# Optimization experiments

Measured on AMD Instinct MI355X. Metric: run time of the kernel, lower is better.

## Reference

```python
import jax, jax.numpy as jnp
import numpy as np
import math

D_K = 64

def setup_inputs() -> dict:
    key = jax.random.key(0)
    k1, k2, k3, k4 = jax.random.split(key, 4)
    B, H, S, D = 2, 16, 2048, D_K
    query = jax.random.normal(k1, (B, H, S, D), dtype=jnp.float32)
    kk = jax.random.normal(k2, (B, H, S, D), dtype=jnp.float32)
    value = jax.random.normal(k3, (B, H, S, D), dtype=jnp.float32)
    mask = jax.random.randint(k4, (B, 1, S, S), 0, 2).astype(bool)
    return {"query": query, "key": kk, "value": value, "mask": mask}

def reference(query, key, value, mask):
    # score = Q K^T / sqrt(d_k)  -> [B,H,S,S]
    score = jnp.einsum('bhqd,bhkd->bhqk', query, key) * (1.0 / math.sqrt(D_K))
    # masked_fill(mask, -inf)
    score = jnp.where(mask, -jnp.inf, score)
    attn = jax.nn.softmax(score, axis=-1)
    # rows that are fully masked produce NaN -> 0 (torch.nan_to_num)
    attn = jnp.nan_to_num(attn, nan=0.0)
    # dropout with drop_rate=0 is identity
    return jnp.einsum('bhqk,bhkd->bhqd', attn, value)
```

## Files before the change

### kernel.cpp

```cpp
#include <hip/hip_runtime.h>
#include <hip/hip_bf16.h>


#define S_LEN 2048
#define D_DIM 64
#define BH    32
#define BM    64
#define BN    64
#define PST   72
#define QSCALE 0.1803368801f

typedef __bf16    bf16_t;
typedef _Float16  f16_t;
typedef bf16_t bf16x8 __attribute__((ext_vector_type(8)));
typedef f16_t  f16x4  __attribute__((ext_vector_type(4)));
typedef float  f32x4  __attribute__((ext_vector_type(4)));
typedef unsigned char  u8;
typedef unsigned long long u64b;

__device__ __forceinline__ void load_lds16(const void* g, void* l) {
    __builtin_amdgcn_global_load_lds(
        (const __attribute__((address_space(1))) void*)g,
        (__attribute__((address_space(3))) void*)l, 16, 0, 0);
}

__global__ __launch_bounds__(256)
void mask_to_bits(const unsigned* __restrict__ M, u64b* __restrict__ bm)
{
    const int t = threadIdx.x;
    unsigned p = M[(t * 8179) & ((1 << 21) - 1)];
    const int is_u8 = __syncthreads_or(p > 1u);
    const int id = blockIdx.x * 256 + t;
    u64b w = 0;
    if (is_u8) {
        const uint4* src = (const uint4*)((const u8*)M + (size_t)id * 64);
        #pragma unroll
        for (int g = 0; g < 4; ++g) {
            uint4 x = src[g];
            const unsigned dw[4] = {x.x, x.y, x.z, x.w};
            #pragma unroll
            for (int q = 0; q < 4; ++q) {
                const unsigned v = dw[q];
                const int base = g * 16 + q * 4;
                if (v & 0x000000FFu) w |= 1ull << (base + 0);
                if (v & 0x0000FF00u) w |= 1ull << (base + 1);
                if (v & 0x00FF0000u) w |= 1ull << (base + 2);
                if (v & 0xFF000000u) w |= 1ull << (base + 3);
            }
        }
    } else {
        const uint4* src = (const uint4*)(M + (size_t)id * 64);
        #pragma unroll
        for (int g = 0; g < 16; ++g) {
            uint4 x = src[g];
            if (x.x) w |= 1ull << (g * 4 + 0);
            if (x.y) w |= 1ull << (g * 4 + 1);
            if (x.z) w |= 1ull << (g * 4 + 2);
            if (x.w) w |= 1ull << (g * 4 + 3);
        }
    }
    bm[id] = w;
}

__global__ __launch_bounds__(256)
void k_prep(const float* __restrict__ K, bf16_t* __restrict__ Kb)
{
    const size_t i = ((size_t)blockIdx.x * 256 + threadIdx.x) * 8;
    float4 a = *(const float4*)(K + i);
    float4 b = *(const float4*)(K + i + 4);
    bf16x8 w;
    w[0]=(bf16_t)a.x; w[1]=(bf16_t)a.y; w[2]=(bf16_t)a.z; w[3]=(bf16_t)a.w;
    w[4]=(bf16_t)b.x; w[5]=(bf16_t)b.y; w[6]=(bf16_t)b.z; w[7]=(bf16_t)b.w;
    const size_t r = i >> 6;
    const int    g = (int)((i & 63) >> 3);
    *(bf16x8*)(Kb + r * 64 + ((g ^ (int)(r & 7)) * 8)) = w;
}

__global__ __launch_bounds__(256)
void v_transpose(const float* __restrict__ V, f16_t* __restrict__ Vt)
{
    __shared__ f16_t T[128][PST];
    const int t  = threadIdx.x;
    const int sc = blockIdx.x;
    const int bh = blockIdx.y;
    const float* Vh = V + ((size_t)bh * S_LEN + sc * 128) * D_DIM;
    #pragma unroll
    for (int it = 0; it < 4; ++it) {
        const int row = it * 32 + (t >> 3);
        const int c8  = (t & 7) * 8;
        float4 a = *(const float4*)(Vh + row * D_DIM + c8);
        float4 b = *(const float4*)(Vh + row * D_DIM + c8 + 4);
        f16_t* d = &T[row][c8];
        d[0]=(f16_t)a.x; d[1]=(f16_t)a.y; d[2]=(f16_t)a.z; d[3]=(f16_t)a.w;
        d[4]=(f16_t)b.x; d[5]=(f16_t)b.y; d[6]=(f16_t)b.z; d[7]=(f16_t)b.w;
    }
    __syncthreads();
    const int d = t >> 2;
    #pragma unroll
    for (int g = 0; g < 4; ++g) {
        const int s_off = (t & 3) * 32 + g * 8;
        const int kbt   = sc * 2 + (s_off >> 6);
        const int k_in  = s_off & 63;
        const int gk    = k_in >> 3;
        f16x4 w0, w1;
        #pragma unroll
        for (int j = 0; j < 4; ++j) { w0[j] = T[s_off + j][d]; w1[j] = T[s_off + 4 + j][d]; }
        f16_t* dst = Vt + (((size_t)bh * (S_LEN/BN) + kbt) * D_DIM + d) * 64
                        + ((gk ^ (d & 7)) * 8);
        *(f16x4*)dst = w0;
        *(f16x4*)(dst + 4) = w1;
    }
}

__global__ __launch_bounds__(256, 4)
void fa_fwd(const float* __restrict__ Q, const float* __restrict__ K,
            const float* __restrict__ V, const void* __restrict__ M,
            const u64b* __restrict__ bm, const bf16_t* __restrict__ Kb,
            const f16_t* __restrict__ Vt, float* __restrict__ O)
{
    __shared__ __align__(16) bf16_t KldsA[BN * D_DIM];
    __shared__ __align__(16) bf16_t KldsB[BN * D_DIM];
    __shared__ __align__(16) f16_t  VldsA[D_DIM * BN];
    __shared__ __align__(16) f16_t  VldsB[D_DIM * BN];

    const int tid  = threadIdx.x;
    const int wave = tid >> 6;
    const int lane = tid & 63;
    const int quad = lane >> 4;
    const int ln   = lane & 15;

    const int qt = blockIdx.x;
    const int bh = blockIdx.y;
    const int b  = bh >> 4;
    const int qbase = qt * BM + wave * 16;

    const size_t head_off = (size_t)bh * S_LEN * D_DIM;
    const float* Qh = Q + head_off;
    const float* Kh = K + head_off;
    const float* Vh = V + head_off;
    const bf16_t* Kbh = Kb ? (Kb + head_off) : nullptr;
    const u8*  Mb8  = (const u8*)M  + (size_t)b * S_LEN * S_LEN;
    const int* Mb32 = (const int*)M + (size_t)b * S_LEN * S_LEN;

    int mask_is_u8 = 0;
    if (!bm) {
        int probe = ((const int*)M)[(tid * 8179) & ((1 << 21) - 1)];
        mask_is_u8 = __syncthreads_or((unsigned)probe > 1u);
    }

    bf16x8 qfrag[2];
    {
        const float* qrow = Qh + (size_t)(qbase + ln) * D_DIM;
        #pragma unroll
        for (int s = 0; s < 2; ++s) {
            float4 a = *(const float4*)(qrow + s * 32 + quad * 8);
            float4 c = *(const float4*)(qrow + s * 32 + quad * 8 + 4);
            bf16x8 w;
            w[0]=(bf16_t)(a.x*QSCALE); w[1]=(bf16_t)(a.y*QSCALE);
            w[2]=(bf16_t)(a.z*QSCALE); w[3]=(bf16_t)(a.w*QSCALE);
            w[4]=(bf16_t)(c.x*QSCALE); w[5]=(bf16_t)(c.y*QSCALE);
            w[6]=(bf16_t)(c.z*QSCALE); w[7]=(bf16_t)(c.w*QSCALE);
            qfrag[s] = w;
        }
    }

    f32x4 accO[4] = {{0.f,0.f,0.f,0.f},{0.f,0.f,0.f,0.f},
                     {0.f,0.f,0.f,0.f},{0.f,0.f,0.f,0.f}};
    float lpart = 0.f;

    const int xg = ln & 7;
    const size_t bmrow = ((size_t)b * S_LEN + qbase + ln) * 32;

    auto load_wm = [&](int kb) -> u64b {
        if (bm) return bm[bmrow + (kb >> 6)];
        u64b w = 0;
        if (mask_is_u8) {
            const u8* mp = Mb8 + (size_t)(qbase + ln) * S_LEN + kb;
            #pragma unroll
            for (int t = 0; t < 4; ++t)
                #pragma unroll
                for (int j = 0; j < 4; ++j) {
                    const int k = t*16 + quad*4 + j;
                    if (mp[k]) w |= 1ull << k;
                }
        } else {
            const int* mp = Mb32 + (size_t)(qbase + ln) * S_LEN + kb;
            #pragma unroll
            for (int t = 0; t < 4; ++t)
                #pragma unroll
                for (int j = 0; j < 4; ++j) {
                    const int k = t*16 + quad*4 + j;
                    if (mp[k]) w |= 1ull << k;
                }
        }
        return w;
    };

    auto prefetch = [&](int kb, bf16_t* Kl, f16_t* Vl) {
        const bf16_t* kt = Kbh + (size_t)kb * D_DIM;
        const f16_t*  vt = Vt + ((size_t)bh * (S_LEN/BN) + (kb >> 6)) * (BN * D_DIM);
        #pragma unroll
        for (int i = 0; i < 2; ++i) {
            const int c = wave + 4 * i;
            load_lds16(kt + c * 512 + lane * 8, Kl + c * 512);
            load_lds16(vt + c * 512 + lane * 8, Vl + c * 512);
        }
    };

    auto compute_tile = [&](const bf16_t* Kl, const f16_t* Vl, u64b wm) {
        f32x4 St[4] = {{0.f,0.f,0.f,0.f},{0.f,0.f,0.f,0.f},
                       {0.f,0.f,0.f,0.f},{0.f,0.f,0.f,0.f}};
        #pragma unroll
        for (int s = 0; s < 2; ++s) {
            #pragma unroll
            for (int t = 0; t < 4; ++t) {
                bf16x8 ak = *(const bf16x8*)
                    &Kl[(16*t + ln) * D_DIM + (((s*4 + quad) ^ xg) * 8)];
                St[t] = __builtin_amdgcn_mfma_f32_16x16x32_bf16(ak, qfrag[s], St[t], 0, 0, 0);
            }
        }
        f16x4 pa[4];
        #pragma unroll
        for (int t = 0; t < 4; ++t) {
            const unsigned nib = (unsigned)(wm >> (t*16 + quad*4)) & 0xFu;
            #pragma unroll
            for (int j = 0; j < 4; ++j) {
                const float p = (nib & (1u << j)) ? 0.f
                              : __builtin_amdgcn_exp2f(St[t][j]);
                lpart += p;
                pa[t][j] = (f16_t)p;
            }
        }
        #pragma unroll
        for (int t = 0; t < 4; ++t) {
            #pragma unroll
            for (int dt = 0; dt < 4; ++dt) {
                const int g = 2*t + (quad >> 1);
                f16x4 bv = *(const f16x4*)
                    &Vl[(dt*16 + ln) * D_DIM + ((g ^ xg) * 8) + (quad & 1) * 4];
                accO[dt] = __builtin_amdgcn_mfma_f32_16x16x16f16(pa[t], bv, accO[dt], 0, 0, 0);
            }
        }
    };

    if (Kbh) {
        prefetch(0, KldsA, VldsA);
        for (int kb = 0; kb < S_LEN; kb += 2 * BN) {
            __syncthreads();
            u64b wm = load_wm(kb);
            if (kb + BN < S_LEN) prefetch(kb + BN, KldsB, VldsB);
            compute_tile(KldsA, VldsA, wm);
            __syncthreads();
            wm = load_wm(kb + BN);
            if (kb + 2*BN < S_LEN) prefetch(kb + 2*BN, KldsA, VldsA);
            compute_tile(KldsB, VldsB, wm);
        }
    } else {
        const int srow = tid >> 2;
        const int sgrp = tid & 3;
        for (int kb = 0; kb < S_LEN; kb += BN) {
            __syncthreads();
            const float* kp = Kh + (size_t)(kb + srow) * D_DIM + sgrp * 16;
            #pragma unroll
            for (int h = 0; h < 2; ++h) {
                float4 a = *(const float4*)(kp + h * 8);
                float4 c = *(const float4*)(kp + h * 8 + 4);
                bf16x8 w;
                w[0]=(bf16_t)a.x; w[1]=(bf16_t)a.y; w[2]=(bf16_t)a.z; w[3]=(bf16_t)a.w;
                w[4]=(bf16_t)c.x; w[5]=(bf16_t)c.y; w[6]=(bf16_t)c.z; w[7]=(bf16_t)c.w;
                const int g = sgrp * 2 + h;
                *(bf16x8*)&KldsA[srow * D_DIM + ((g ^ (srow & 7)) * 8)] = w;
            }
            const float* vp = Vh + (size_t)(kb + srow) * D_DIM + sgrp * 16;
            float vv[16];
            #pragma unroll
            for (int g = 0; g < 4; ++g) {
                float4 a = *(const float4*)(vp + g * 4);
                vv[g*4+0]=a.x; vv[g*4+1]=a.y; vv[g*4+2]=a.z; vv[g*4+3]=a.w;
            }
            const int gk = srow >> 3;
            #pragma unroll
            for (int jj = 0; jj < 16; ++jj) {
                const int j = (jj + srow) & 15;
                const int d = sgrp * 16 + j;
                VldsA[d * D_DIM + ((gk ^ (d & 7)) * 8) + (srow & 7)] = (f16_t)vv[j];
            }
            __syncthreads();
            compute_tile(KldsA, VldsA, load_wm(kb));
        }
    }

    lpart += __shfl_xor(lpart, 16, 64);
    lpart += __shfl_xor(lpart, 32, 64);
    #pragma unroll
    for (int r = 0; r < 4; ++r) {
        const float lr  = __shfl(lpart, quad * 4 + r, 64);
        const float inv = (lr > 0.f) ? 1.f / lr : 0.f;
        float* orow = O + head_off + (size_t)(qbase + quad*4 + r) * D_DIM;
        #pragma unroll
        for (int dt = 0; dt < 4; ++dt)
            orow[16*dt + ln] = accO[dt][r] * inv;
    }
}

extern "C" void kernel_launch(void* const* d_in, const int* in_sizes, int n_in,
                              void* d_out, int out_size, void* d_ws, size_t ws_size,
                              hipStream_t stream) {
    (void)in_sizes; (void)n_in; (void)out_size;
    const float* Q = (const float*)d_in[0];
    const float* K = (const float*)d_in[1];
    const float* V = (const float*)d_in[2];
    const void*  M = d_in[3];
    float* O = (float*)d_out;

    const size_t bm_bytes = (size_t)2 * S_LEN * (S_LEN / 64) * 8;
    const size_t kv_elems = (size_t)BH * S_LEN * D_DIM;
    const size_t need_all = bm_bytes + 2 * kv_elems * 2;

    u64b*   bm = (ws_size >= bm_bytes) ? (u64b*)d_ws : nullptr;
    bf16_t* Kb = nullptr; f16_t* Vt = nullptr;
    if (ws_size >= need_all) {
        Kb = (bf16_t*)((char*)d_ws + bm_bytes);
        Vt = (f16_t*)(Kb + kv_elems);
    }

    if (bm)
        mask_to_bits<<<dim3(131072 / 256), dim3(256), 0, stream>>>(
            (const unsigned*)M, bm);
    if (Kb) {
        k_prep<<<dim3((unsigned)(kv_elems / 8 / 256)), dim3(256), 0, stream>>>(K, Kb);
        v_transpose<<<dim3(S_LEN / 128, BH), dim3(256), 0, stream>>>(V, Vt);
    }

    dim3 grid(S_LEN / BM, BH);
    fa_fwd<<<grid, dim3(256), 0, stream>>>(Q, K, V, M, bm, Kb, Vt, O);
}
```

Before: 182.3 us.

## Use 16x16x32 f16 MFMA for PV with permuted K rows and mask-init scores

After: 302.3 us. 65.8% more time.

```diff
diff --git a/kernel.cpp b/kernel.cpp
--- a/kernel.cpp
+++ b/kernel.cpp
@@ -13,7 +13,9 @@
 typedef __bf16    bf16_t;
 typedef _Float16  f16_t;
 typedef bf16_t bf16x8 __attribute__((ext_vector_type(8)));
+typedef f16_t  f16x2  __attribute__((ext_vector_type(2)));
 typedef f16_t  f16x4  __attribute__((ext_vector_type(4)));
+typedef f16_t  f16x8  __attribute__((ext_vector_type(8)));
 typedef float  f32x4  __attribute__((ext_vector_type(4)));
 typedef unsigned char  u8;
 typedef unsigned long long u64b;
@@ -22,6 +24,14 @@
     __builtin_amdgcn_global_load_lds(
         (const __attribute__((address_space(1))) void*)g,
         (__attribute__((address_space(3))) void*)l, 16, 0, 0);
+}
+
+__device__ __forceinline__ f16x2 cvt_pk_f16(float a, float b) {
+    return __builtin_bit_cast(f16x2, __builtin_amdgcn_cvt_pkrtz(a, b));
+}
+
+__device__ __forceinline__ int fswf(int r) {
+    return (r & 3) | (((r >> 3) & 1) << 2);
 }
 
 __global__ __launch_bounds__(256)
@@ -73,7 +83,7 @@
     w[4]=(bf16_t)b.x; w[5]=(bf16_t)b.y; w[6]=(bf16_t)b.z; w[7]=(bf16_t)b.w;
     const size_t r = i >> 6;
     const int    g = (int)((i & 63) >> 3);
-    *(bf16x8*)(Kb + r * 64 + ((g ^ (int)(r & 7)) * 8)) = w;
+    *(bf16x8*)(Kb + r * 64 + ((g ^ fswf((int)(r & 63))) * 8)) = w;
 }
 
 __global__ __launch_bounds__(256)
@@ -129,9 +139,10 @@
     const int quad = lane >> 4;
     const int ln   = lane & 15;
 
-    const int qt = blockIdx.x;
-    const int bh = blockIdx.y;
-    const int b  = bh >> 4;
+    const int lin = (int)blockIdx.y * 32 + (int)blockIdx.x;
+    const int qt  = (lin >> 3) & 31;
+    const int bh  = ((lin & 7) << 2) | (lin >> 8);
+    const int b   = bh >> 4;
     const int qbase = qt * BM + wave * 16;
 
     const size_t head_off = (size_t)bh * S_LEN * D_DIM;
@@ -168,7 +179,24 @@
                      {0.f,0.f,0.f,0.f},{0.f,0.f,0.f,0.f}};
     float lpart = 0.f;
 
-    const int xg = ln & 7;
+    const int fswl = (ln & 3) | (((ln >> 2) & 1) << 2);
+    const int xv   = ln & 7;
+    int koff[2][4];
+    #pragma unroll
+    for (int s = 0; s < 2; ++s)
+      #pragma unroll
+      for (int T = 0; T < 2; ++T)
+        #pragma unroll
+        for (int u = 0; u < 2; ++u)
+            koff[s][2*T+u] = (32*T + (ln >> 2) * 8 + 4*u + (ln & 3)) * D_DIM
+                           + (((s*4 + quad) ^ fswl) * 8);
+    int voff[2][4];
+    #pragma unroll
+    for (int T = 0; T < 2; ++T)
+      #pragma unroll
+      for (int dt = 0; dt < 4; ++dt)
+            voff[T][dt] = (dt*16 + ln) * D_DIM + (((T*4 + quad) ^ xv) * 8);
+
     const size_t bmrow = ((size_t)b * S_LEN + qbase + ln) * 32;
 
     auto load_wm = [&](int kb) -> u64b {
@@ -177,19 +205,19 @@
         if (mask_is_u8) {
             const u8* mp = Mb8 + (size_t)(qbase + ln) * S_LEN + kb;
             #pragma unroll
-            for (int t = 0; t < 4; ++t)
+            for (int t2 = 0; t2 < 2; ++t2)
                 #pragma unroll
-                for (int j = 0; j < 4; ++j) {
-                    const int k = t*16 + quad*4 + j;
+                for (int j = 0; j < 8; ++j) {
+                    const int k = t2*32 + quad*8 + j;
                     if (mp[k]) w |= 1ull << k;
                 }
         } else {
             const int* mp = Mb32 + (size_t)(qbase + ln) * S_LEN + kb;
             #pragma unroll
-            for (int t = 0; t < 4; ++t)
+            for (int t2 = 0; t2 < 2; ++t2)
                 #pragma unroll
-                for (int j = 0; j < 4; ++j) {
-                    const int k = t*16 + quad*4 + j;
+                for (int j = 0; j < 8; ++j) {
+                    const int k = t2*32 + quad*8 + j;
                     if (mp[k]) w |= 1ull << k;
                 }
         }
@@ -208,52 +236,64 @@
     };
 
     auto compute_tile = [&](const bf16_t* Kl, const f16_t* Vl, u64b wm) {
-        f32x4 St[4] = {{0.f,0.f,0.f,0.f},{0.f,0.f,0.f,0.f},
-                       {0.f,0.f,0.f,0.f},{0.f,0.f,0.f,0.f}};
-        #pragma unroll
-        for (int s = 0; s < 2; ++s) {
-            #pragma unroll
-            for (int t = 0; t < 4; ++t) {
-                bf16x8 ak = *(const bf16x8*)
-                    &Kl[(16*t + ln) * D_DIM + (((s*4 + quad) ^ xg) * 8)];
-                St[t] = __builtin_amdgcn_mfma_f32_16x16x32_bf16(ak, qfrag[s], St[t], 0, 0, 0);
-            }
-        }
-        f16x4 pa[4];
-        #pragma unroll
-        for (int t = 0; t < 4; ++t) {
-            const unsigned nib = (unsigned)(wm >> (t*16 + quad*4)) & 0xFu;
-            #pragma unroll
-            for (int j = 0; j < 4; ++j) {
-                const float p = (nib & (1u << j)) ? 0.f
-                              : __builtin_amdgcn_exp2f(St[t][j]);
-                lpart += p;
-                pa[t][j] = (f16_t)p;
-            }
-        }
-        #pragma unroll
-        for (int t = 0; t < 4; ++t) {
+        f32x4 St[4];
+        #pragma unroll
+        for (int T = 0; T < 2; ++T)
+          #pragma unroll
+          for (int u = 0; u < 2; ++u) {
+            const unsigned nib = (unsigned)(wm >> (T*32 + quad*8 + u*4)) & 0xFu;
+            f32x4 iv;
+            #pragma unroll
+            for (int j = 0; j < 4; ++j)
+                iv[j] = (nib & (1u << j)) ? -512.f : 0.f;
+            St[2*T + u] = iv;
+          }
+        __builtin_amdgcn_s_setprio(1);
+        #pragma unroll
+        for (int s = 0; s < 2; ++s)
+          #pragma unroll
+          for (int t = 0; t < 4; ++t) {
+            bf16x8 ak = *(const bf16x8*)(Kl + koff[s][t]);
+            St[t] = __builtin_amdgcn_mfma_f32_16x16x32_bf16(ak, qfrag[s], St[t], 0, 0, 0);
+          }
+        __builtin_amdgcn_s_setprio(0);
+        #pragma unroll
+        for (int T = 0; T < 2; ++T) {
+            f16x2 h[4];
+            #pragma unroll
+            for (int u = 0; u < 2; ++u)
+              #pragma unroll
+              for (int jj = 0; jj < 2; ++jj) {
+                const float e0 = __builtin_amdgcn_exp2f(St[2*T+u][2*jj]);
+                const float e1 = __builtin_amdgcn_exp2f(St[2*T+u][2*jj+1]);
+                lpart += e0 + e1;
+                h[u*2+jj] = cvt_pk_f16(e0, e1);
+              }
+            const f16x8 pa = {h[0][0], h[0][1], h[1][0], h[1][1],
+                              h[2][0], h[2][1], h[3][0], h[3][1]};
+            __builtin_amdgcn_s_setprio(1);
             #pragma unroll
             for (int dt = 0; dt < 4; ++dt) {
-                const int g = 2*t + (quad >> 1);
-                f16x4 bv = *(const f16x4*)
-                    &Vl[(dt*16 + ln) * D_DIM + ((g ^ xg) * 8) + (quad & 1) * 4];
-                accO[dt] = __builtin_amdgcn_mfma_f32_16x16x16f16(pa[t], bv, accO[dt], 0, 0, 0);
-            }
+                f16x8 bv = *(const f16x8*)(Vl + voff[T][dt]);
+                accO[dt] = __builtin_amdgcn_mfma_f32_16x16x32_f16(pa, bv, accO[dt], 0, 0, 0);
+            }
+            __builtin_amdgcn_s_setprio(0);
         }
     };
 
     if (Kbh) {
         prefetch(0, KldsA, VldsA);
+        u64b wmA = load_wm(0);
         for (int kb = 0; kb < S_LEN; kb += 2 * BN) {
             __syncthreads();
-            u64b wm = load_wm(kb);
+            u64b wmB = load_wm(kb + BN);
             if (kb + BN < S_LEN) prefetch(kb + BN, KldsB, VldsB);
-            compute_tile(KldsA, VldsA, wm);
+            compute_tile(KldsA, VldsA, wmA);
             __syncthreads();
-            wm = load_wm(kb + BN);
+            const int kn = (kb + 2*BN < S_LEN) ? (kb + 2*BN) : 0;
+            wmA = load_wm(kn);
             if (kb + 2*BN < S_LEN) prefetch(kb + 2*BN, KldsA, VldsA);
-            compute_tile(KldsB, VldsB, wm);
+            compute_tile(KldsB, VldsB, wmB);
         }
     } else {
         const int srow = tid >> 2;
@@ -269,7 +309,7 @@
                 w[0]=(bf16_t)a.x; w[1]=(bf16_t)a.y; w[2]=(bf16_t)a.z; w[3]=(bf16_t)a.w;
                 w[4]=(bf16_t)c.x; w[5]=(bf16_t)c.y; w[6]=(bf16_t)c.z; w[7]=(bf16_t)c.w;
                 const int g = sgrp * 2 + h;
-                *(bf16x8*)&KldsA[srow * D_DIM + ((g ^ (srow & 7)) * 8)] = w;
+                *(bf16x8*)&KldsA[srow * D_DIM + ((g ^ fswf(srow)) * 8)] = w;
             }
             const float* vp = Vh + (size_t)(kb + srow) * D_DIM + sgrp * 16;
             float vv[16];
```

## Fuse mask, K and V prepass kernels into one launch; add MFMA wave priority

Applied to the files above, without the earlier changes.

After: 176.7 us (median of 2 runs). -3.1%, faster.

```diff
diff --git a/kernel.cpp b/kernel.cpp
--- a/kernel.cpp
+++ b/kernel.cpp
@@ -63,52 +63,93 @@
 }
 
 __global__ __launch_bounds__(256)
-void k_prep(const float* __restrict__ K, bf16_t* __restrict__ Kb)
+void prepass_all(const unsigned* __restrict__ M, u64b* __restrict__ bm,
+                 const float* __restrict__ K, bf16_t* __restrict__ Kb,
+                 const float* __restrict__ V, f16_t* __restrict__ Vt)
 {
-    const size_t i = ((size_t)blockIdx.x * 256 + threadIdx.x) * 8;
-    float4 a = *(const float4*)(K + i);
-    float4 b = *(const float4*)(K + i + 4);
-    bf16x8 w;
-    w[0]=(bf16_t)a.x; w[1]=(bf16_t)a.y; w[2]=(bf16_t)a.z; w[3]=(bf16_t)a.w;
-    w[4]=(bf16_t)b.x; w[5]=(bf16_t)b.y; w[6]=(bf16_t)b.z; w[7]=(bf16_t)b.w;
-    const size_t r = i >> 6;
-    const int    g = (int)((i & 63) >> 3);
-    *(bf16x8*)(Kb + r * 64 + ((g ^ (int)(r & 7)) * 8)) = w;
-}
-
-__global__ __launch_bounds__(256)
-void v_transpose(const float* __restrict__ V, f16_t* __restrict__ Vt)
-{
-    __shared__ f16_t T[128][PST];
-    const int t  = threadIdx.x;
-    const int sc = blockIdx.x;
-    const int bh = blockIdx.y;
-    const float* Vh = V + ((size_t)bh * S_LEN + sc * 128) * D_DIM;
+    const int t   = threadIdx.x;
+    const int blk = blockIdx.x;
+
+    unsigned p = M[(t * 8179) & ((1 << 21) - 1)];
+    const int is_u8 = __syncthreads_or(p > 1u);
+
+    {
+        const int id = blk * 256 + t;
+        u64b w = 0;
+        if (is_u8) {
+            const uint4* src = (const uint4*)((const u8*)M + (size_t)id * 64);
+            #pragma unroll
+            for (int g = 0; g < 4; ++g) {
+                uint4 x = src[g];
+                const unsigned dw[4] = {x.x, x.y, x.z, x.w};
+                #pragma unroll
+                for (int q = 0; q < 4; ++q) {
+                    const unsigned v = dw[q];
+                    const int base = g * 16 + q * 4;
+                    if (v & 0x000000FFu) w |= 1ull << (base + 0);
+                    if (v & 0x0000FF00u) w |= 1ull << (base + 1);
+                    if (v & 0x00FF0000u) w |= 1ull << (base + 2);
+                    if (v & 0xFF000000u) w |= 1ull << (base + 3);
+                }
+            }
+        } else {
+            const uint4* src = (const uint4*)(M + (size_t)id * 64);
+            #pragma unroll
+            for (int g = 0; g < 16; ++g) {
+                uint4 x = src[g];
+                if (x.x) w |= 1ull << (g * 4 + 0);
+                if (x.y) w |= 1ull << (g * 4 + 1);
+                if (x.z) w |= 1ull << (g * 4 + 2);
+                if (x.w) w |= 1ull << (g * 4 + 3);
+            }
+        }
+        bm[id] = w;
+    }
+
     #pragma unroll
-    for (int it = 0; it < 4; ++it) {
-        const int row = it * 32 + (t >> 3);
-        const int c8  = (t & 7) * 8;
-        float4 a = *(const float4*)(Vh + row * D_DIM + c8);
-        float4 b = *(const float4*)(Vh + row * D_DIM + c8 + 4);
-        f16_t* d = &T[row][c8];
-        d[0]=(f16_t)a.x; d[1]=(f16_t)a.y; d[2]=(f16_t)a.z; d[3]=(f16_t)a.w;
-        d[4]=(f16_t)b.x; d[5]=(f16_t)b.y; d[6]=(f16_t)b.z; d[7]=(f16_t)b.w;
-    }
-    __syncthreads();
-    const int d = t >> 2;
-    #pragma unroll
-    for (int g = 0; g < 4; ++g) {
-        const int s_off = (t & 3) * 32 + g * 8;
-        const int kbt   = sc * 2 + (s_off >> 6);
-        const int k_in  = s_off & 63;
-        const int gk    = k_in >> 3;
-        f16x4 w0, w1;
-        #pragma unroll
-        for (int j = 0; j < 4; ++j) { w0[j] = T[s_off + j][d]; w1[j] = T[s_off + 4 + j][d]; }
-        f16_t* dst = Vt + (((size_t)bh * (S_LEN/BN) + kbt) * D_DIM + d) * 64
-                        + ((gk ^ (d & 7)) * 8);
-        *(f16x4*)dst = w0;
-        *(f16x4*)(dst + 4) = w1;
+    for (int j = 0; j < 4; ++j) {
+        const size_t i = ((size_t)(blk * 256 + t) + (size_t)j * 131072) * 8;
+        float4 a = *(const float4*)(K + i);
+        float4 b = *(const float4*)(K + i + 4);
+        bf16x8 w;
+        w[0]=(bf16_t)a.x; w[1]=(bf16_t)a.y; w[2]=(bf16_t)a.z; w[3]=(bf16_t)a.w;
+        w[4]=(bf16_t)b.x; w[5]=(bf16_t)b.y; w[6]=(bf16_t)b.z; w[7]=(bf16_t)b.w;
+        const size_t r = i >> 6;
+        const int    g = (int)((i & 63) >> 3);
+        *(bf16x8*)(Kb + r * 64 + ((g ^ (int)(r & 7)) * 8)) = w;
+    }
+
+    {
+        __shared__ f16_t T[128][PST];
+        const int sc = blk & 15;
+        const int bh = blk >> 4;
+        const float* Vh = V + ((size_t)bh * S_LEN + sc * 128) * D_DIM;
+        #pragma unroll
+        for (int it = 0; it < 4; ++it) {
+            const int row = it * 32 + (t >> 3);
+            const int c8  = (t & 7) * 8;
+            float4 a = *(const float4*)(Vh + row * D_DIM + c8);
+            float4 b = *(const float4*)(Vh + row * D_DIM + c8 + 4);
+            f16_t* d = &T[row][c8];
+            d[0]=(f16_t)a.x; d[1]=(f16_t)a.y; d[2]=(f16_t)a.z; d[3]=(f16_t)a.w;
+            d[4]=(f16_t)b.x; d[5]=(f16_t)b.y; d[6]=(f16_t)b.z; d[7]=(f16_t)b.w;
+        }
+        __syncthreads();
+        const int d = t >> 2;
+        #pragma unroll
+        for (int g = 0; g < 4; ++g) {
+            const int s_off = (t & 3) * 32 + g * 8;
+            const int kbt   = sc * 2 + (s_off >> 6);
+            const int k_in  = s_off & 63;
+            const int gk    = k_in >> 3;
+            f16x4 w0, w1;
+            #pragma unroll
+            for (int j = 0; j < 4; ++j) { w0[j] = T[s_off + j][d]; w1[j] = T[s_off + 4 + j][d]; }
+            f16_t* dst = Vt + (((size_t)bh * (S_LEN/BN) + kbt) * D_DIM + d) * 64
+                            + ((gk ^ (d & 7)) * 8);
+            *(f16x4*)dst = w0;
+            *(f16x4*)(dst + 4) = w1;
+        }
     }
 }
 
@@ -210,6 +251,7 @@
     auto compute_tile = [&](const bf16_t* Kl, const f16_t* Vl, u64b wm) {
         f32x4 St[4] = {{0.f,0.f,0.f,0.f},{0.f,0.f,0.f,0.f},
                        {0.f,0.f,0.f,0.f},{0.f,0.f,0.f,0.f}};
+        __builtin_amdgcn_s_setprio(1);
         #pragma unroll
         for (int s = 0; s < 2; ++s) {
             #pragma unroll
@@ -219,6 +261,7 @@
                 St[t] = __builtin_amdgcn_mfma_f32_16x16x32_bf16(ak, qfrag[s], St[t], 0, 0, 0);
             }
         }
+        __builtin_amdgcn_s_setprio(0);
         f16x4 pa[4];
         #pragma unroll
         for (int t = 0; t < 4; ++t) {
@@ -231,6 +274,7 @@
                 pa[t][j] = (f16_t)p;
             }
         }
+        __builtin_amdgcn_s_setprio(1);
         #pragma unroll
         for (int t = 0; t < 4; ++t) {
             #pragma unroll
@@ -241,6 +285,7 @@
                 accO[dt] = __builtin_amdgcn_mfma_f32_16x16x16f16(pa[t], bv, accO[dt], 0, 0, 0);
             }
         }
+        __builtin_amdgcn_s_setprio(0);
     };
 
     if (Kbh) {
@@ -324,12 +369,12 @@
         Vt = (f16_t*)(Kb + kv_elems);
     }
 
-    if (bm)
+    if (bm && Kb) {
+        prepass_all<<<dim3(512), dim3(256), 0, stream>>>(
+            (const unsigned*)M, bm, K, Kb, V, Vt);
+    } else if (bm) {
         mask_to_bits<<<dim3(131072 / 256), dim3(256), 0, stream>>>(
             (const unsigned*)M, bm);
-    if (Kb) {
-        k_prep<<<dim3((unsigned)(kv_elems / 8 / 256)), dim3(256), 0, stream>>>(K, Kb);
-        v_transpose<<<dim3(S_LEN / 128, BH), dim3(256), 0, stream>>>(V, Vt);
     }
 
     dim3 grid(S_LEN / BM, BH);
```
